# Performance work log

Measured on AMD Instinct MI355X. Metric: run time of the kernel, lower is better.

## Reference

```python
import jax, jax.numpy as jnp
import numpy as np

B, T, D_S, D_H, D_ATT = 64, 2048, 512, 512, 512


def setup_inputs() -> dict:
    key = jax.random.key(0)
    ks = jax.random.split(key, 6)
    scale_s = 1.0 / np.sqrt(D_S)
    scale_h = 1.0 / np.sqrt(D_H)
    return {
        "s": jax.random.normal(ks[0], (B, D_S), dtype=jnp.float32),
        "h": jax.random.normal(ks[1], (B, T, D_H), dtype=jnp.float32),
        "phi_w": jax.random.normal(ks[2], (D_ATT, D_S), dtype=jnp.float32) * scale_s,
        "phi_b": jax.random.normal(ks[3], (D_ATT,), dtype=jnp.float32) * scale_s,
        "psi_w": jax.random.normal(ks[4], (D_ATT, D_H), dtype=jnp.float32) * scale_h,
        "psi_b": jax.random.normal(ks[5], (D_ATT,), dtype=jnp.float32) * scale_h,
    }


def reference(s, h, phi_w, phi_b, psi_w, psi_b):
    # phi(s): [B, d_att]; psi(h): [B, T, d_att]
    phi_s = s @ phi_w.T + phi_b
    psi_h = jnp.einsum('bth,ah->bta', h, psi_w) + psi_b
    # scores e[b,t] = sum_a phi_s[b,a] * psi_h[b,t,a]
    e = jnp.einsum('ba,bta->bt', phi_s, psi_h)
    alpha = jax.nn.softmax(e, axis=-1)  # [B, T]
    # faithful to original: 'ij,ijk->ij' sums h over feature dim k
    c = alpha * h.sum(axis=-1)  # [B, T]
    return c
```

## Files before the change

### kernel.cpp

```cpp
#include <hip/hip_runtime.h>
#include <math.h>

#define B 64
#define T 2048
#define DS 512
#define DH 512
#define DA 512

typedef float fx4 __attribute__((ext_vector_type(4)));
typedef float fx2 __attribute__((ext_vector_type(2)));

__global__ __launch_bounds__(256) void k_phiv(const float* __restrict__ s,
                                              const float* __restrict__ phi_w,
                                              const float* __restrict__ phi_b,
                                              const float* __restrict__ psi_w,
                                              float* __restrict__ vp) {
    __shared__ float phi_part[DA / 4];
    const int b = blockIdx.x >> 2;
    const int q = blockIdx.x & 3;
    const int tid  = threadIdx.x;
    const int wave = tid >> 6;
    const int lane = tid & 63;

    const fx4* s4 = (const fx4*)(s + (size_t)b * DS);
    const fx4 sA = s4[lane * 2], sB = s4[lane * 2 + 1];

    for (int i = 0; i < 32; ++i) {
        const int a_local = wave * 32 + i;
        const int a = q * (DA / 4) + a_local;
        const fx4* w4 = (const fx4*)(phi_w + (size_t)a * DS);
        const fx4 wA = w4[lane * 2], wB = w4[lane * 2 + 1];
        float acc = sA.x * wA.x + sA.y * wA.y + sA.z * wA.z + sA.w * wA.w
                  + sB.x * wB.x + sB.y * wB.y + sB.z * wB.z + sB.w * wB.w;
        #pragma unroll
        for (int off = 32; off > 0; off >>= 1)
            acc += __shfl_down(acc, off, 64);
        if (lane == 0) phi_part[a_local] = acc + phi_b[a];
    }
    __syncthreads();

    const fx2* w2 = (const fx2*)psi_w;
    fx2 acc = {0.f, 0.f};
    #pragma unroll 8
    for (int a = 0; a < DA / 4; ++a) {
        const float p = phi_part[a];
        acc += p * w2[(size_t)(q * (DA / 4) + a) * (DH / 2) + tid];
    }
    ((fx2*)(vp + ((size_t)q * B + b) * DH))[tid] = acc;
}

__global__ __launch_bounds__(256) void k_scores(const float* __restrict__ h,
                                                const float* __restrict__ vp,
                                                float* __restrict__ e,
                                                float* __restrict__ rs) {
    __shared__ float vsum[DH];
    const int tid  = threadIdx.x;
    const int base = blockIdx.x * 16;
    const int b    = base >> 11;

    {
        fx2 acc = {0.f, 0.f};
        #pragma unroll
        for (int q = 0; q < 4; ++q) {
            const fx2* v2 = (const fx2*)(vp + ((size_t)q * B + b) * DH);
            acc += v2[tid];
        }
        ((fx2*)vsum)[tid] = acc;
    }
    __syncthreads();

    const int wave = tid >> 6;
    const int lane = tid & 63;
    const fx4 vA = ((const fx4*)vsum)[lane * 2];
    const fx4 vB = ((const fx4*)vsum)[lane * 2 + 1];

    const int row0 = base + wave * 4;
    fx4 hA[4], hB[4];
    #pragma unroll
    for (int r = 0; r < 4; ++r) {
        const fx4* h4 = (const fx4*)(h + (size_t)(row0 + r) * DH);
        hA[r] = __builtin_nontemporal_load(&h4[lane * 2]);
        hB[r] = __builtin_nontemporal_load(&h4[lane * 2 + 1]);
    }

    float dot[4], sum[4];
    #pragma unroll
    for (int r = 0; r < 4; ++r) {
        dot[r] = hA[r].x * vA.x + hA[r].y * vA.y + hA[r].z * vA.z + hA[r].w * vA.w
               + hB[r].x * vB.x + hB[r].y * vB.y + hB[r].z * vB.z + hB[r].w * vB.w;
        sum[r] = hA[r].x + hA[r].y + hA[r].z + hA[r].w
               + hB[r].x + hB[r].y + hB[r].z + hB[r].w;
    }
    #pragma unroll
    for (int off = 32; off > 0; off >>= 1) {
        #pragma unroll
        for (int r = 0; r < 4; ++r) {
            dot[r] += __shfl_down(dot[r], off, 64);
            sum[r] += __shfl_down(sum[r], off, 64);
        }
    }
    if (lane == 0) {
        #pragma unroll
        for (int r = 0; r < 4; ++r) { e[row0 + r] = dot[r]; rs[row0 + r] = sum[r]; }
    }
}

__global__ __launch_bounds__(256) void k_softmax(const float* __restrict__ e,
                                                 const float* __restrict__ rs,
                                                 float* __restrict__ c) {
    __shared__ float wred[4];
    const int b = blockIdx.x;
    const int tid  = threadIdx.x;
    const int wave = tid >> 6;
    const int lane = tid & 63;
    const fx4* eb = (const fx4*)(e + (size_t)b * T);

    fx4 evA = eb[tid * 2], evB = eb[tid * 2 + 1];

    float m = fmaxf(fmaxf(fmaxf(evA.x, evA.y), fmaxf(evA.z, evA.w)),
                    fmaxf(fmaxf(evB.x, evB.y), fmaxf(evB.z, evB.w)));
    #pragma unroll
    for (int off = 32; off > 0; off >>= 1)
        m = fmaxf(m, __shfl_down(m, off, 64));
    if (lane == 0) wred[wave] = m;
    __syncthreads();
    m = fmaxf(fmaxf(wred[0], wred[1]), fmaxf(wred[2], wred[3]));

    evA.x = expf(evA.x - m); evA.y = expf(evA.y - m);
    evA.z = expf(evA.z - m); evA.w = expf(evA.w - m);
    evB.x = expf(evB.x - m); evB.y = expf(evB.y - m);
    evB.z = expf(evB.z - m); evB.w = expf(evB.w - m);
    float lsum = evA.x + evA.y + evA.z + evA.w + evB.x + evB.y + evB.z + evB.w;
    #pragma unroll
    for (int off = 32; off > 0; off >>= 1)
        lsum += __shfl_down(lsum, off, 64);
    __syncthreads();
    if (lane == 0) wred[wave] = lsum;
    __syncthreads();
    const float inv = 1.0f / (wred[0] + wred[1] + wred[2] + wred[3]);

    const fx4* rb = (const fx4*)(rs + (size_t)b * T);
    fx4* cb = (fx4*)(c + (size_t)b * T);
    fx4 rA = rb[tid * 2], rB = rb[tid * 2 + 1];
    fx4 oA, oB;
    oA.x = evA.x * inv * rA.x; oA.y = evA.y * inv * rA.y;
    oA.z = evA.z * inv * rA.z; oA.w = evA.w * inv * rA.w;
    oB.x = evB.x * inv * rB.x; oB.y = evB.y * inv * rB.y;
    oB.z = evB.z * inv * rB.z; oB.w = evB.w * inv * rB.w;
    cb[tid * 2] = oA;
    cb[tid * 2 + 1] = oB;
}

extern "C" void kernel_launch(void* const* d_in, const int* in_sizes, int n_in,
                              void* d_out, int out_size, void* d_ws, size_t ws_size,
                              hipStream_t stream) {
    const float* s     = (const float*)d_in[0];
    const float* h     = (const float*)d_in[1];
    const float* phi_w = (const float*)d_in[2];
    const float* phi_b = (const float*)d_in[3];
    const float* psi_w = (const float*)d_in[4];
    (void)in_sizes; (void)n_in; (void)out_size; (void)ws_size;

    float* out = (float*)d_out;
    float* ws  = (float*)d_ws;
    float* vp    = ws;
    float* e     = vp + 4 * B * DH;
    float* rs    = e + B * T;

    k_phiv   <<<B * 4,      256, 0, stream>>>(s, phi_w, phi_b, psi_w, vp);
    k_scores <<<B * T / 16, 256, 0, stream>>>(h, vp, e, rs);
    k_softmax<<<B,          256, 0, stream>>>(e, rs, out);
}
```

Baseline: 386.6 us.

## Split phi projection into a separate highly parallel kernel before the v projection

Splits the fused phi/v kernel in two. The phi projection now runs as its own kernel with one wave per output element across many blocks, replacing the serial 32-iteration loop per wave. The v projection reads phi from workspace using 128-thread blocks and float4 loads of psi_w. This is meant to cut the latency of the serialized phi stage, at the cost of an extra kernel launch and a round trip of phi through global memory.

```diff
diff --git a/kernel.cpp b/kernel.cpp
--- a/kernel.cpp
+++ b/kernel.cpp
@@ -10,43 +10,47 @@
 typedef float fx4 __attribute__((ext_vector_type(4)));
 typedef float fx2 __attribute__((ext_vector_type(2)));
 
-__global__ __launch_bounds__(256) void k_phiv(const float* __restrict__ s,
-                                              const float* __restrict__ phi_w,
-                                              const float* __restrict__ phi_b,
-                                              const float* __restrict__ psi_w,
-                                              float* __restrict__ vp) {
-    __shared__ float phi_part[DA / 4];
+__global__ __launch_bounds__(256) void k_phi(const float* __restrict__ s,
+                                             const float* __restrict__ phi_w,
+                                             const float* __restrict__ phi_b,
+                                             float* __restrict__ phi_s) {
+    const int wave = threadIdx.x >> 6;
+    const int lane = threadIdx.x & 63;
+    const int out  = blockIdx.x * 4 + wave;
+    const int b = out >> 9;
+    const int a = out & 511;
+
+    const fx4* s4 = (const fx4*)(s + (size_t)b * DS);
+    const fx4* w4 = (const fx4*)(phi_w + (size_t)a * DS);
+    fx4 sA = s4[lane * 2], sB = s4[lane * 2 + 1];
+    fx4 wA = w4[lane * 2], wB = w4[lane * 2 + 1];
+    float acc = sA.x * wA.x + sA.y * wA.y + sA.z * wA.z + sA.w * wA.w
+              + sB.x * wB.x + sB.y * wB.y + sB.z * wB.z + sB.w * wB.w;
+    #pragma unroll
+    for (int off = 32; off > 0; off >>= 1)
+        acc += __shfl_down(acc, off, 64);
+    if (lane == 0) phi_s[out] = acc + phi_b[a];
+}
+
+__global__ __launch_bounds__(128) void k_v(const float* __restrict__ phi_s,
+                                           const float* __restrict__ psi_w,
+                                           float* __restrict__ vp) {
+    __shared__ float ps[DA / 4];
     const int b = blockIdx.x >> 2;
     const int q = blockIdx.x & 3;
-    const int tid  = threadIdx.x;
-    const int wave = tid >> 6;
-    const int lane = tid & 63;
-
-    const fx4* s4 = (const fx4*)(s + (size_t)b * DS);
-    const fx4 sA = s4[lane * 2], sB = s4[lane * 2 + 1];
-
-    for (int i = 0; i < 32; ++i) {
-        const int a_local = wave * 32 + i;
-        const int a = q * (DA / 4) + a_local;
-        const fx4* w4 = (const fx4*)(phi_w + (size_t)a * DS);
-        const fx4 wA = w4[lane * 2], wB = w4[lane * 2 + 1];
-        float acc = sA.x * wA.x + sA.y * wA.y + sA.z * wA.z + sA.w * wA.w
-                  + sB.x * wB.x + sB.y * wB.y + sB.z * wB.z + sB.w * wB.w;
-        #pragma unroll
-        for (int off = 32; off > 0; off >>= 1)
-            acc += __shfl_down(acc, off, 64);
-        if (lane == 0) phi_part[a_local] = acc + phi_b[a];
-    }
+    const int tid = threadIdx.x;
+    ps[tid] = phi_s[(size_t)b * DA + q * (DA / 4) + tid];
     __syncthreads();
 
-    const fx2* w2 = (const fx2*)psi_w;
-    fx2 acc = {0.f, 0.f};
+    const fx4* w4 = (const fx4*)psi_w;
+    fx4 acc = {0.f, 0.f, 0.f, 0.f};
     #pragma unroll 8
     for (int a = 0; a < DA / 4; ++a) {
-        const float p = phi_part[a];
-        acc += p * w2[(size_t)(q * (DA / 4) + a) * (DH / 2) + tid];
+        const float p = ps[a];
+        const fx4 w = w4[(q * (DA / 4) + a) * (DH / 4) + tid];
+        acc += p * w;
     }
-    ((fx2*)(vp + ((size_t)q * B + b) * DH))[tid] = acc;
+    ((fx4*)(vp + ((size_t)q * B + b) * DH))[tid] = acc;
 }
 
 __global__ __launch_bounds__(256) void k_scores(const float* __restrict__ h,
@@ -163,11 +167,13 @@
 
     float* out = (float*)d_out;
     float* ws  = (float*)d_ws;
-    float* vp    = ws;
+    float* phi_s = ws;
+    float* vp    = phi_s + B * DA;
     float* e     = vp + 4 * B * DH;
     float* rs    = e + B * T;
 
-    k_phiv   <<<B * 4,      256, 0, stream>>>(s, phi_w, phi_b, psi_w, vp);
+    k_phi    <<<B * DA / 4, 256, 0, stream>>>(s, phi_w, phi_b, phi_s);
+    k_v      <<<B * 4,      128, 0, stream>>>(phi_s, psi_w, vp);
     k_scores <<<B * T / 16, 256, 0, stream>>>(h, vp, e, rs);
     k_softmax<<<B,          256, 0, stream>>>(e, rs, out);
 }
```

Result: faster. 373.8 us (-3.3%).
